# Kernel optimization log

Hardware: AMD Instinct MI355X
Metric: run time of the kernel (lower is better)

Reference implementation:

```python
import jax, jax.numpy as jnp
import numpy as np

SR = 16000
NFFT = 512
NFILT = 64
FRAME_LEN = 400    # 0.025 * 16000
FRAME_STEP = 160   # 0.010 * 16000
NUM_FRAMES = 50000


def _mel_filterbanks():
    # python_speech_features get_filterbanks(nfilt=64, nfft=512, sr=16000, lowfreq=0, highfreq=sr/2)
    def hz2mel(hz):
        return 2595.0 * np.log10(1.0 + hz / 700.0)

    def mel2hz(m):
        return 700.0 * (10.0 ** (m / 2595.0) - 1.0)

    highfreq = SR / 2.0
    melpts = np.linspace(hz2mel(0.0), hz2mel(highfreq), NFILT + 2)
    bins = np.floor((NFFT + 1) * mel2hz(melpts) / SR)
    fb = np.zeros((NFILT, NFFT // 2 + 1), dtype=np.float64)
    for j in range(NFILT):
        for i in range(int(bins[j]), int(bins[j + 1])):
            fb[j, i] = (i - bins[j]) / (bins[j + 1] - bins[j])
        for i in range(int(bins[j + 1]), int(bins[j + 2])):
            fb[j, i] = (bins[j + 2] - i) / (bins[j + 2] - bins[j + 1])
    return fb.T.astype(np.float32)  # (257, nfilt) == filters.T in the original


def setup_inputs() -> dict:
    key = jax.random.key(0)
    audio_len = FRAME_LEN + (NUM_FRAMES - 1) * FRAME_STEP  # 8_000_240 -> exactly 50000 frames, zero pad
    x = jax.random.normal(key, (1, audio_len), dtype=jnp.float32)
    filters = jnp.asarray(_mel_filterbanks())
    return {"x": x, "filters": filters}


def reference(x, filters):
    # pre-emphasis
    x = jnp.concatenate([x[:, :1], x[:, 1:] - 0.97 * x[:, :-1]], axis=1)
    audio_len = x.shape[1]
    num_frames = (audio_len - FRAME_LEN) // FRAME_STEP + 1
    # vectorized framing (replaces the per-frame python slice/stack loop)
    idx = jnp.arange(num_frames)[:, None] * FRAME_STEP + jnp.arange(FRAME_LEN)[None, :]
    windowed = x[:, idx]                                     # (B, F, frame_len)
    r = jnp.fft.rfft(windowed, n=NFFT, axis=2)               # (B, F, nfft//2+1)
    power = (jnp.real(r) ** 2 + jnp.imag(r) ** 2) * (1.0 / NFFT)
    feat = jnp.einsum('bfk,kn->bfn', power, filters) + 1e-30  # (B, F, nfilt)
    # per-frame normalization over (batch, filters), matching reduce_mean/K.std on feat[:, i, :]
    m = jnp.mean(feat, axis=(0, 2), keepdims=True)
    s = jnp.std(feat, axis=(0, 2), keepdims=True)
    feat = (feat - m) / s
    return feat[..., None]                                   # (1, F, nfilt, 1)
```

## Files before the change

### kernel.cpp

```cpp
#include <hip/hip_runtime.h>
#include <math.h>

#define NFILT 64
#define FRAME_LEN 400
#define FRAME_STEP 160
#define WMAX 24
#define WSTRIDE 25
#define WAVES 4
#define NBLOCKS 1563
#define PWBINS 280

__global__ __launch_bounds__(256) void fbank_kernel(const float* __restrict__ x,
                                                    const float* __restrict__ filters,
                                                    float* __restrict__ out,
                                                    int num_frames) {
    __shared__ float wc_lds[NFILT * WSTRIDE];
    __shared__ int   lo_lds[NFILT];
    __shared__ float pw[WAVES][PWBINS * 2];

    const int t = threadIdx.x;
    const int l = t & 63;
    const int w = t >> 6;
    float* pwrow = pw[w];

    if (l < 2 * (PWBINS - 257)) pwrow[2 * 257 + l] = 0.0f;

    if (w == 0) {
        int lo = 257;
        for (int k = 0; k < 257; k++) {
            float fv = filters[k * NFILT + l];
            if (fv != 0.0f && lo == 257) lo = k;
        }
        if (lo > 256) lo = 256;
        lo_lds[l] = lo;
        for (int i = 0; i < WMAX; i++) {
            int k = lo + i;
            wc_lds[l * WSTRIDE + i] = (k <= 256) ? filters[k * NFILT + l] : 0.0f;
        }
    }

    const int rl = (int)(__brev((unsigned)l) >> 26);
    float cA[6], sA[6], sg[6];
#pragma unroll
    for (int j = 0; j < 6; j++) {
        const int d = 32 >> j;
        const int hi = l & d;
        float th = -2.0f * (float)M_PI * (float)(l & (d - 1)) / (float)(2 * d);
        cA[j] = hi ? cosf(th) : 1.0f;
        sA[j] = hi ? sinf(th) : 0.0f;
        sg[j] = hi ? -1.0f : 1.0f;
    }
    float br[8], bi[8];
    {
        float th = -2.0f * (float)M_PI * (float)rl * (1.0f / 512.0f);
        float c1 = cosf(th), s1 = sinf(th);
        br[0] = 1.0f; bi[0] = 0.0f; br[1] = c1; bi[1] = s1;
#pragma unroll
        for (int r = 2; r < 8; r++) {
            float pr_ = br[r - 1], pi_ = bi[r - 1];
            br[r] = pr_ * c1 - pi_ * s1;
            bi[r] = pr_ * s1 + pi_ * c1;
        }
    }
    const int Lp = (int)(__brev((unsigned)((64 - rl) & 63)) >> 26);

    __syncthreads();
    const int lo = lo_lds[l];

    const int gw = blockIdx.x * WAVES + w;
    const int totw = gridDim.x * WAVES;
    const int npairs = (num_frames + 1) >> 1;

    for (int pair = gw; pair < npairs; pair += totw) {
        const long fa = 2L * pair;
        const bool hasb = (fa + 1) < num_frames;
        const long ba = fa * FRAME_STEP;
        const long bb = ba + FRAME_STEP;

        float vr[8], vi[8];
        {
            float a0=0,a1=0,a2=0,a3=0,a4=0,a5=0,a6=0,a7=0;
            if (l < 50) {
                const float4* p4 = reinterpret_cast<const float4*>(x + ba + 8 * l);
                float4 A = p4[0], B = p4[1];
                a0=A.x; a1=A.y; a2=A.z; a3=A.w; a4=B.x; a5=B.y; a6=B.z; a7=B.w;
            }
            float ev = x[ba > 0 ? ba - 1 : 0];
            float edge = (ba > 0) ? ev : 0.0f;
            float prev = __shfl_up(a7, 1, 64);
            if (l == 0) prev = edge;
            vr[0] = (l < 50) ? fmaf(-0.97f, prev, a0) : 0.0f;
            vr[1] = (l < 50) ? fmaf(-0.97f, a0, a1) : 0.0f;
            vr[2] = (l < 50) ? fmaf(-0.97f, a1, a2) : 0.0f;
            vr[3] = (l < 50) ? fmaf(-0.97f, a2, a3) : 0.0f;
            vr[4] = (l < 50) ? fmaf(-0.97f, a3, a4) : 0.0f;
            vr[5] = (l < 50) ? fmaf(-0.97f, a4, a5) : 0.0f;
            vr[6] = (l < 50) ? fmaf(-0.97f, a5, a6) : 0.0f;
            vr[7] = (l < 50) ? fmaf(-0.97f, a6, a7) : 0.0f;
        }
        {
            float b0=0,b1=0,b2=0,b3=0,b4=0,b5=0,b6=0,b7=0;
            if (hasb && l < 50) {
                const float4* p4 = reinterpret_cast<const float4*>(x + bb + 8 * l);
                float4 A = p4[0], B = p4[1];
                b0=A.x; b1=A.y; b2=A.z; b3=A.w; b4=B.x; b5=B.y; b6=B.z; b7=B.w;
            }
            float edge = hasb ? x[bb - 1] : 0.0f;
            float prev = __shfl_up(b7, 1, 64);
            if (l == 0) prev = edge;
            vi[0] = (l < 50) ? fmaf(-0.97f, prev, b0) : 0.0f;
            vi[1] = (l < 50) ? fmaf(-0.97f, b0, b1) : 0.0f;
            vi[2] = (l < 50) ? fmaf(-0.97f, b1, b2) : 0.0f;
            vi[3] = (l < 50) ? fmaf(-0.97f, b2, b3) : 0.0f;
            vi[4] = (l < 50) ? fmaf(-0.97f, b3, b4) : 0.0f;
            vi[5] = (l < 50) ? fmaf(-0.97f, b4, b5) : 0.0f;
            vi[6] = (l < 50) ? fmaf(-0.97f, b5, b6) : 0.0f;
            vi[7] = (l < 50) ? fmaf(-0.97f, b6, b7) : 0.0f;
        }

#pragma unroll
        for (int j = 0; j < 6; j++) {
            const int d = 32 >> j;
            const float c = cA[j], s = sA[j], g = sg[j];
#pragma unroll
            for (int r = 0; r < 8; r++) {
                float pr = __shfl_xor(vr[r], d, 64);
                float pi = __shfl_xor(vi[r], d, 64);
                float tr = fmaf(g, vr[r], pr);
                float ti = fmaf(g, vi[r], pi);
                vr[r] = tr * c - ti * s;
                vi[r] = tr * s + ti * c;
            }
        }

#pragma unroll
        for (int r = 1; r < 8; r++) {
            float tr = vr[r], ti = vi[r];
            vr[r] = tr * br[r] - ti * bi[r];
            vi[r] = tr * bi[r] + ti * br[r];
        }

        const float RH = 0.70710678118654752f;
        {
            float t0r=vr[0]+vr[4], t0i=vi[0]+vi[4];
            float d0r=vr[0]-vr[4], d0i=vi[0]-vi[4];
            float t1r=vr[1]+vr[5], t1i=vi[1]+vi[5];
            float d1r=vr[1]-vr[5], d1i=vi[1]-vi[5];
            float t2r=vr[2]+vr[6], t2i=vi[2]+vi[6];
            float d2r=vr[2]-vr[6], d2i=vi[2]-vi[6];
            float t3r=vr[3]+vr[7], t3i=vi[3]+vi[7];
            float d3r=vr[3]-vr[7], d3i=vi[3]-vi[7];
            vr[0]=t0r; vi[0]=t0i; vr[1]=t1r; vi[1]=t1i;
            vr[2]=t2r; vi[2]=t2i; vr[3]=t3r; vi[3]=t3i;
            vr[4]=d0r;                 vi[4]=d0i;
            vr[5]=(d1r+d1i)*RH;        vi[5]=(d1i-d1r)*RH;
            vr[6]=d2i;                 vi[6]=-d2r;
            vr[7]=(d3i-d3r)*RH;        vi[7]=-(d3r+d3i)*RH;
        }
        {
            float t0r=vr[0]+vr[2], t0i=vi[0]+vi[2];
            float d0r=vr[0]-vr[2], d0i=vi[0]-vi[2];
            float t1r=vr[1]+vr[3], t1i=vi[1]+vi[3];
            float d1r=vr[1]-vr[3], d1i=vi[1]-vi[3];
            vr[0]=t0r; vi[0]=t0i; vr[1]=t1r; vi[1]=t1i;
            vr[2]=d0r; vi[2]=d0i; vr[3]=d1i; vi[3]=-d1r;
            float t4r=vr[4]+vr[6], t4i=vi[4]+vi[6];
            float d4r=vr[4]-vr[6], d4i=vi[4]-vi[6];
            float t5r=vr[5]+vr[7], t5i=vi[5]+vi[7];
            float d5r=vr[5]-vr[7], d5i=vi[5]-vi[7];
            vr[4]=t4r; vi[4]=t4i; vr[5]=t5r; vi[5]=t5i;
            vr[6]=d4r; vi[6]=d4i; vr[7]=d5i; vi[7]=-d5r;
        }
        {
            float t0r=vr[0]+vr[1], t0i=vi[0]+vi[1];
            float d0r=vr[0]-vr[1], d0i=vi[0]-vi[1];
            vr[0]=t0r; vi[0]=t0i; vr[1]=d0r; vi[1]=d0i;
            float t2r=vr[2]+vr[3], t2i=vi[2]+vi[3];
            float d2r=vr[2]-vr[3], d2i=vi[2]-vi[3];
            vr[2]=t2r; vi[2]=t2i; vr[3]=d2r; vi[3]=d2i;
            float t4r=vr[4]+vr[5], t4i=vi[4]+vi[5];
            float d4r=vr[4]-vr[5], d4i=vi[4]-vi[5];
            vr[4]=t4r; vi[4]=t4i; vr[5]=d4r; vi[5]=d4i;
            float t6r=vr[6]+vr[7], t6i=vi[6]+vi[7];
            float d6r=vr[6]-vr[7], d6i=vi[6]-vi[7];
            vr[6]=t6r; vi[6]=t6i; vr[7]=d6r; vi[7]=d6i;
        }

        float c0r = __shfl(vr[7], Lp, 64), c0i = __shfl(vi[7], Lp, 64);
        float c1r = __shfl(vr[3], Lp, 64), c1i = __shfl(vi[3], Lp, 64);
        float c2r = __shfl(vr[5], Lp, 64), c2i = __shfl(vi[5], Lp, 64);
        float c3r = __shfl(vr[1], Lp, 64), c3i = __shfl(vi[1], Lp, 64);
        if (l == 0) {
            c0r = vr[0]; c0i = vi[0];
            c1r = vr[7]; c1i = vi[7];
            c2r = vr[3]; c2i = vi[3];
            c3r = vr[5]; c3i = vi[5];
        }

        const float S4 = (1.0f / 512.0f) * 0.25f;
        {
            float zr = vr[0], zi = vi[0];
            float e1 = zr + c0r, e2 = zi - c0i, o1 = zi + c0i, o2 = c0r - zr;
            float2 pq = make_float2((e1*e1 + e2*e2) * S4, (o1*o1 + o2*o2) * S4);
            *reinterpret_cast<float2*>(&pwrow[2 * rl]) = pq;
        }
        {
            float zr = vr[4], zi = vi[4];
            float e1 = zr + c1r, e2 = zi - c1i, o1 = zi + c1i, o2 = c1r - zr;
            float2 pq = make_float2((e1*e1 + e2*e2) * S4, (o1*o1 + o2*o2) * S4);
            *reinterpret_cast<float2*>(&pwrow[2 * (rl + 64)]) = pq;
        }
        {
            float zr = vr[2], zi = vi[2];
            float e1 = zr + c2r, e2 = zi - c2i, o1 = zi + c2i, o2 = c2r - zr;
            float2 pq = make_float2((e1*e1 + e2*e2) * S4, (o1*o1 + o2*o2) * S4);
            *reinterpret_cast<float2*>(&pwrow[2 * (rl + 128)]) = pq;
        }
        {
            float zr = vr[6], zi = vi[6];
            float e1 = zr + c3r, e2 = zi - c3i, o1 = zi + c3i, o2 = c3r - zr;
            float2 pq = make_float2((e1*e1 + e2*e2) * S4, (o1*o1 + o2*o2) * S4);
            *reinterpret_cast<float2*>(&pwrow[2 * (rl + 192)]) = pq;
        }
        if (l == 0) {
            pwrow[512] = vr[1] * vr[1] * (1.0f / 512.0f);
            pwrow[513] = vi[1] * vi[1] * (1.0f / 512.0f);
        }

        asm volatile("s_waitcnt lgkmcnt(0)" ::: "memory");

        float acca = 1e-30f, accb = 1e-30f;
#pragma unroll
        for (int i = 0; i < WMAX; i++) {
            float wv = wc_lds[l * WSTRIDE + i];
            float2 pq = *reinterpret_cast<const float2*>(&pwrow[2 * (lo + i)]);
            acca = fmaf(wv, pq.x, acca);
            accb = fmaf(wv, pq.y, accb);
        }

        float sa = acca, sb = accb;
#pragma unroll
        for (int mk = 1; mk < 64; mk <<= 1) {
            sa += __shfl_xor(sa, mk, 64);
            sb += __shfl_xor(sb, mk, 64);
        }
        const float ma = sa * (1.0f / 64.0f), mb = sb * (1.0f / 64.0f);
        const float da = acca - ma, db = accb - mb;
        float va = da * da, vb = db * db;
#pragma unroll
        for (int mk = 1; mk < 64; mk <<= 1) {
            va += __shfl_xor(va, mk, 64);
            vb += __shfl_xor(vb, mk, 64);
        }
        out[fa * NFILT + l] = da / sqrtf(va * (1.0f / 64.0f));
        if (hasb)
            out[(fa + 1) * NFILT + l] = db / sqrtf(vb * (1.0f / 64.0f));
    }
}

extern "C" void kernel_launch(void* const* d_in, const int* in_sizes, int n_in,
                              void* d_out, int out_size, void* d_ws, size_t ws_size,
                              hipStream_t stream) {
    (void)d_ws; (void)ws_size; (void)n_in; (void)in_sizes;
    const float* x = (const float*)d_in[0];
    const float* filters = (const float*)d_in[1];
    float* out = (float*)d_out;
    const int num_frames = out_size / NFILT;
    fbank_kernel<<<NBLOCKS, 256, 0, stream>>>(x, filters, out, num_frames);
}
```

Before: 102.5 us.

## Launch one wave per frame pair and cheapen setup math

The grid grows so each wave handles roughly one frame pair instead of looping over several. The per-block filter scan for the first nonzero bin is unrolled with batched loads. Twiddle setup switches to the fast intrinsics __cosf/__sinf, and the final normalization uses rsqrtf multiplies instead of divide-by-sqrt. The larger grid repeats the filter-table setup in every block, and the fast trig and rsqrt intrinsics may change results slightly.

```diff
diff --git a/kernel.cpp b/kernel.cpp
--- a/kernel.cpp
+++ b/kernel.cpp
@@ -2,12 +2,11 @@
 #include <math.h>
 
 #define NFILT 64
-#define FRAME_LEN 400
 #define FRAME_STEP 160
 #define WMAX 24
 #define WSTRIDE 25
 #define WAVES 4
-#define NBLOCKS 1563
+#define NBLOCKS 6250
 #define PWBINS 280
 
 __global__ __launch_bounds__(256) void fbank_kernel(const float* __restrict__ x,
@@ -27,9 +26,18 @@
 
     if (w == 0) {
         int lo = 257;
-        for (int k = 0; k < 257; k++) {
-            float fv = filters[k * NFILT + l];
-            if (fv != 0.0f && lo == 257) lo = k;
+#pragma unroll 4
+        for (int k0 = 0; k0 < 264; k0 += 8) {
+            float fv[8];
+#pragma unroll
+            for (int i = 0; i < 8; i++) {
+                int k = k0 + i;
+                fv[i] = (k < 257) ? filters[k * NFILT + l] : 0.0f;
+            }
+#pragma unroll
+            for (int i = 0; i < 8; i++) {
+                if (fv[i] != 0.0f && lo == 257) lo = k0 + i;
+            }
         }
         if (lo > 256) lo = 256;
         lo_lds[l] = lo;
@@ -46,14 +54,14 @@
         const int d = 32 >> j;
         const int hi = l & d;
         float th = -2.0f * (float)M_PI * (float)(l & (d - 1)) / (float)(2 * d);
-        cA[j] = hi ? cosf(th) : 1.0f;
-        sA[j] = hi ? sinf(th) : 0.0f;
+        cA[j] = hi ? __cosf(th) : 1.0f;
+        sA[j] = hi ? __sinf(th) : 0.0f;
         sg[j] = hi ? -1.0f : 1.0f;
     }
     float br[8], bi[8];
     {
         float th = -2.0f * (float)M_PI * (float)rl * (1.0f / 512.0f);
-        float c1 = cosf(th), s1 = sinf(th);
+        float c1 = __cosf(th), s1 = __sinf(th);
         br[0] = 1.0f; bi[0] = 0.0f; br[1] = c1; bi[1] = s1;
 #pragma unroll
         for (int r = 2; r < 8; r++) {
@@ -68,7 +76,7 @@
     const int lo = lo_lds[l];
 
     const int gw = blockIdx.x * WAVES + w;
-    const int totw = gridDim.x * WAVES;
+    const int totw = NBLOCKS * WAVES;
     const int npairs = (num_frames + 1) >> 1;
 
     for (int pair = gw; pair < npairs; pair += totw) {
@@ -201,26 +209,26 @@
         {
             float zr = vr[0], zi = vi[0];
             float e1 = zr + c0r, e2 = zi - c0i, o1 = zi + c0i, o2 = c0r - zr;
-            float2 pq = make_float2((e1*e1 + e2*e2) * S4, (o1*o1 + o2*o2) * S4);
-            *reinterpret_cast<float2*>(&pwrow[2 * rl]) = pq;
+            *reinterpret_cast<float2*>(&pwrow[2 * rl]) =
+                make_float2((e1*e1 + e2*e2) * S4, (o1*o1 + o2*o2) * S4);
         }
         {
             float zr = vr[4], zi = vi[4];
             float e1 = zr + c1r, e2 = zi - c1i, o1 = zi + c1i, o2 = c1r - zr;
-            float2 pq = make_float2((e1*e1 + e2*e2) * S4, (o1*o1 + o2*o2) * S4);
-            *reinterpret_cast<float2*>(&pwrow[2 * (rl + 64)]) = pq;
+            *reinterpret_cast<float2*>(&pwrow[2 * (rl + 64)]) =
+                make_float2((e1*e1 + e2*e2) * S4, (o1*o1 + o2*o2) * S4);
         }
         {
             float zr = vr[2], zi = vi[2];
             float e1 = zr + c2r, e2 = zi - c2i, o1 = zi + c2i, o2 = c2r - zr;
-            float2 pq = make_float2((e1*e1 + e2*e2) * S4, (o1*o1 + o2*o2) * S4);
-            *reinterpret_cast<float2*>(&pwrow[2 * (rl + 128)]) = pq;
+            *reinterpret_cast<float2*>(&pwrow[2 * (rl + 128)]) =
+                make_float2((e1*e1 + e2*e2) * S4, (o1*o1 + o2*o2) * S4);
         }
         {
             float zr = vr[6], zi = vi[6];
             float e1 = zr + c3r, e2 = zi - c3i, o1 = zi + c3i, o2 = c3r - zr;
-            float2 pq = make_float2((e1*e1 + e2*e2) * S4, (o1*o1 + o2*o2) * S4);
-            *reinterpret_cast<float2*>(&pwrow[2 * (rl + 192)]) = pq;
+            *reinterpret_cast<float2*>(&pwrow[2 * (rl + 192)]) =
+                make_float2((e1*e1 + e2*e2) * S4, (o1*o1 + o2*o2) * S4);
         }
         if (l == 0) {
             pwrow[512] = vr[1] * vr[1] * (1.0f / 512.0f);
@@ -252,9 +260,9 @@
             va += __shfl_xor(va, mk, 64);
             vb += __shfl_xor(vb, mk, 64);
         }
-        out[fa * NFILT + l] = da / sqrtf(va * (1.0f / 64.0f));
+        out[fa * NFILT + l] = da * rsqrtf(va * (1.0f / 64.0f));
         if (hasb)
-            out[(fa + 1) * NFILT + l] = db / sqrtf(vb * (1.0f / 64.0f));
+            out[(fa + 1) * NFILT + l] = db * rsqrtf(vb * (1.0f / 64.0f));
     }
 }
 
```

Result: slower. 258.7 us (+152.5%).
